# Kernel tuning notes

Hardware: AMD Instinct MI355X
Metric: run time of the kernel (lower is better)

Reference implementation:

```python
import jax, jax.numpy as jnp
import numpy as np
from jax import lax

B = 100000      # number of time steps (outer 'batch' loop in the torch code)
SEQ = 1         # inner seq_len
SPIN = 365      # spinLen
TRAIN = 50000   # traintimeLen


def setup_inputs() -> dict:
    key = jax.random.key(0)
    k1, k2, k3, k4, k5 = jax.random.split(key, 5)
    x = jax.random.uniform(k1, (B, SEQ, 2), dtype=jnp.float32)          # [batch, seq, 2] (batch_first)
    y_obs = jax.random.uniform(k2, (B, 1), dtype=jnp.float32)
    weight_r_yom = jax.random.uniform(k3, (1, 1), dtype=jnp.float32)
    weight_r_ylm = jax.random.uniform(k4, (1, 1), dtype=jnp.float32)
    weight_r_yfm = jax.random.uniform(k5, (1, 1), dtype=jnp.float32)
    return {"x": x, "y_obs": y_obs, "weight_r_yom": weight_r_yom,
            "weight_r_ylm": weight_r_ylm, "weight_r_yfm": weight_r_yfm,
            "epoch": 0, "time_lag": 0}


def reference(x, y_obs, weight_r_yom, weight_r_ylm, weight_r_yfm, epoch, time_lag):
    batch_size = x.shape[0]
    dtype = x.dtype
    # obs std over training window (torch.std is unbiased -> ddof=1)
    obsstd = jnp.std(y_obs[SPIN:TRAIN], ddof=1)

    # gates from softmax over the three scalar weights (constant over time)
    ew = jnp.exp(jnp.stack([weight_r_yom, weight_r_ylm, weight_r_yfm]))  # [3,1,1]
    denom = ew.sum(0)
    oo = ew[0] / denom   # (1,1) outflow gate
    ol = ew[1] / denom   # (1,1) loss (ET) gate

    def time_step(c0, u):
        # c0: (1,1) cell state; u: (2,) = (precip u1, PET u2)
        u1, u2 = u[0], u[1]
        safe_c = jnp.where(c0 > 0, c0, jnp.asarray(1.0, dtype))
        olc_raw = jnp.where(c0 > 0, ol - jax.nn.elu(ol - u2 / safe_c), ol)
        f = jax.nn.relu(1.0 - oo - olc_raw)          # forget gate uses pre-relu constraint
        olc = jax.nn.relu(olc_raw)
        c1 = f * c0 + u1                              # ib = 0 -> full input
        outs = (oo * c0, c0, ol * c0, olc * c0, olc, f)
        return c1, outs

    def batch_step(c0, u_seq):
        # u_seq: [SEQ, 2]; stored outputs correspond to the LAST inner t step
        c1, outs = lax.scan(time_step, c0, u_seq)
        return c1, tuple(o[-1] for o in outs)

    c_init = jnp.zeros((1, 1), dtype=dtype)
    _, (q, c, l, lc, g_olc, g_f) = lax.scan(batch_step, c_init, x[time_lag:])

    def pad(a):
        a = a.reshape(-1, 1)
        return jnp.concatenate([jnp.zeros((time_lag, 1), dtype), a], axis=0)

    h_n = pad(q)                     # bp = ib*g = 0, so h_n == q_n == oo*c0
    c_n = pad(c)
    l_n = pad(l)
    lc_n = pad(lc)
    Gate_olc = pad(g_olc)
    Gate_f = pad(g_f)

    tail = jnp.concatenate([jnp.zeros((time_lag, 1), dtype),
                            jnp.ones((batch_size - time_lag, 1), dtype)], axis=0)
    Gate_oo = oo[0, 0] * tail
    Gate_ol = ol[0, 0] * tail
    obs_std = obsstd * tail

    zeros = jnp.zeros((batch_size, 1), dtype)
    bp_n = zeros
    Gate_ib = zeros
    h_nout = jnp.concatenate([h_n, obs_std], axis=1)

    return (h_n, c_n, l_n, lc_n, bp_n, Gate_ib, Gate_oo, Gate_ol,
            Gate_olc, Gate_f, h_nout, obs_std)
```

## Files before the change

### kernel.cpp

```cpp
#include <hip/hip_runtime.h>
#include <math.h>

#define NB    100000
#define TRAIN 50000
#define SPIN  365
#define WARM  64
#define TPB   256
#define SCAN_BLKS ((NB + TPB - 1) / TPB)
#define RED_BLKS  64
#define WIN   (TPB + WARM)

#define V4_BASE  368
#define V4_COUNT 12408

__global__ __launch_bounds__(TPB) void k_all(const float* __restrict__ x,
                                             const float* __restrict__ y_obs,
                                             const float* __restrict__ w0,
                                             const float* __restrict__ w1,
                                             const float* __restrict__ w2,
                                             float* __restrict__ out) {
    const int tid = threadIdx.x;

    if (blockIdx.x < RED_BLKS) {
        __shared__ double ssum[TPB];
        __shared__ double ssq[TPB];
        const int b   = blockIdx.x;
        const int gid = b * TPB + tid;

        double s = 0.0, q = 0.0;
        if (gid < V4_COUNT) {
            const float4 v = ((const float4*)(y_obs + V4_BASE))[gid];
            s = (double)v.x + (double)v.y + (double)v.z + (double)v.w;
            q = (double)v.x * v.x + (double)v.y * v.y
              + (double)v.z * v.z + (double)v.w * v.w;
        }
        if (b == 0 && tid == 0) {
            for (int i = SPIN; i < V4_BASE; ++i) {
                double v = (double)y_obs[i];
                s += v; q += v * v;
            }
        }
        ssum[tid] = s;
        ssq[tid]  = q;
        __syncthreads();
        for (int off = TPB / 2; off > 0; off >>= 1) {
            if (tid < off) {
                ssum[tid] += ssum[tid + off];
                ssq[tid]  += ssq[tid + off];
            }
            __syncthreads();
        }
        __syncthreads();
        double fs = 0.0, fq = 0.0;
        {
            const float4* y4 = (const float4*)(y_obs + V4_BASE);
            for (int i = tid; i < V4_COUNT; i += TPB) {
                float4 v = y4[i];
                fs += (double)v.x + (double)v.y + (double)v.z + (double)v.w;
                fq += (double)v.x * v.x + (double)v.y * v.y
                    + (double)v.z * v.z + (double)v.w * v.w;
            }
            if (tid == 0) {
                for (int i = SPIN; i < V4_BASE; ++i) {
                    double v = (double)y_obs[i];
                    fs += v; fq += v * v;
                }
            }
        }
        __syncthreads();
        ssum[tid] = fs;
        ssq[tid]  = fq;
        __syncthreads();
        for (int off = TPB / 2; off > 0; off >>= 1) {
            if (tid < off) {
                ssum[tid] += ssum[tid + off];
                ssq[tid]  += ssq[tid + off];
            }
            __syncthreads();
        }
        const double n    = (double)(TRAIN - SPIN);
        const double mean = ssum[0] / n;
        const double var  = (ssq[0] - n * mean * mean) / (n - 1.0);
        const float  stdv = (float)sqrt(var);

        float* __restrict__ o_std = out + 12 * NB;
        float* __restrict__ o_hn  = out + 10 * NB;
        const int nth = RED_BLKS * TPB;
        for (int i = b * TPB + tid; i < NB; i += nth) {
            o_std[i]        = stdv;
            o_hn[2 * i + 1] = stdv;
        }
    } else {
        __shared__ float su1[WIN];
        __shared__ float su2[WIN];
        const int b = blockIdx.x - RED_BLKS;
        const int t = b * TPB + tid;

        float e0 = expf(w0[0]);
        float e1 = expf(w1[0]);
        float e2 = expf(w2[0]);
        float denom = e0 + e1 + e2;
        const float oo   = e0 / denom;
        const float ol   = e1 / denom;
        const float omoo = 1.0f - oo;

        const int w0i = max(0, b * TPB - WARM);
        const int r1  = min(NB, b * TPB + TPB);
        const int n4  = (r1 - w0i) >> 1;
        if (tid < n4) {
            const float4 v = ((const float4*)(((const float2*)x) + w0i))[tid];
            su1[2 * tid]     = v.x;  su2[2 * tid]     = v.y;
            su1[2 * tid + 1] = v.z;  su2[2 * tid + 1] = v.w;
        }
        __syncthreads();

        if (t >= NB) return;

        int   wstart = max(0, t - WARM);
        float c = (wstart == 0) ? 0.0f : 1.0f;
        for (int it = wstart; it < t; ++it) {
            float u1 = su1[it - w0i];
            float u2 = su2[it - w0i];
            float r  = __builtin_amdgcn_rcpf(c);
            float z  = ol - u2 * r;
            float el = (z > 0.0f) ? z : (__expf(z) - 1.0f);
            float praw    = ol - el;
            float olc_raw = (c > 0.0f) ? praw : ol;
            float f  = fmaxf(omoo - olc_raw, 0.0f);
            c = fmaf(f, c, u1);
        }
        float u2 = su2[t - w0i];
        float r  = __builtin_amdgcn_rcpf(c);
        float z  = ol - u2 * r;
        float el = (z > 0.0f) ? z : (__expf(z) - 1.0f);
        float praw    = ol - el;
        float olc_raw = (c > 0.0f) ? praw : ol;
        float f   = fmaxf(omoo - olc_raw, 0.0f);
        float olc = fmaxf(olc_raw, 0.0f);
        float h   = oo * c;

        out[0  * NB + t]     = h;
        out[1  * NB + t]     = c;
        out[2  * NB + t]     = ol * c;
        out[3  * NB + t]     = olc * c;
        out[4  * NB + t]     = 0.0f;
        out[5  * NB + t]     = 0.0f;
        out[6  * NB + t]     = oo;
        out[7  * NB + t]     = ol;
        out[8  * NB + t]     = olc;
        out[9  * NB + t]     = f;
        out[10 * NB + 2*t]   = h;
    }
}

extern "C" void kernel_launch(void* const* d_in, const int* in_sizes, int n_in,
                              void* d_out, int out_size, void* d_ws, size_t ws_size,
                              hipStream_t stream) {
    const float* x     = (const float*)d_in[0];
    const float* y_obs = (const float*)d_in[1];
    const float* w0    = (const float*)d_in[2];
    const float* w1    = (const float*)d_in[3];
    const float* w2    = (const float*)d_in[4];
    float* out = (float*)d_out;

    k_all<<<RED_BLKS + SCAN_BLKS, TPB, 0, stream>>>(x, y_obs, w0, w1, w2, out);
}
```

Baseline: 80.44 us.

## Split std reduction into per-block partials plus a finalize kernel

Before, each of the 64 reduction blocks redundantly re-read the whole training window to compute the full std, then wrote the std broadcast outputs. Now each block writes only its partial sum and sum of squares to workspace. A second kernel reduces the 64 partials with wavefront shuffles and writes the std columns. This removes the 64x redundant global reads and reductions but adds a second kernel launch and a dependency between the two kernels.

Result: faster. 73.90 us (-8.1%).

```diff
diff --git a/kernel.cpp b/kernel.cpp
--- a/kernel.cpp
+++ b/kernel.cpp
@@ -13,12 +13,14 @@
 #define V4_BASE  368
 #define V4_COUNT 12408
 
-__global__ __launch_bounds__(TPB) void k_all(const float* __restrict__ x,
-                                             const float* __restrict__ y_obs,
-                                             const float* __restrict__ w0,
-                                             const float* __restrict__ w1,
-                                             const float* __restrict__ w2,
-                                             float* __restrict__ out) {
+
+__global__ __launch_bounds__(TPB) void k_main(const float* __restrict__ x,
+                                              const float* __restrict__ y_obs,
+                                              const float* __restrict__ w0,
+                                              const float* __restrict__ w1,
+                                              const float* __restrict__ w2,
+                                              float* __restrict__ ws,
+                                              float* __restrict__ out) {
     const int tid = threadIdx.x;
 
     if (blockIdx.x < RED_BLKS) {
@@ -50,45 +52,10 @@
             }
             __syncthreads();
         }
-        __syncthreads();
-        double fs = 0.0, fq = 0.0;
-        {
-            const float4* y4 = (const float4*)(y_obs + V4_BASE);
-            for (int i = tid; i < V4_COUNT; i += TPB) {
-                float4 v = y4[i];
-                fs += (double)v.x + (double)v.y + (double)v.z + (double)v.w;
-                fq += (double)v.x * v.x + (double)v.y * v.y
-                    + (double)v.z * v.z + (double)v.w * v.w;
-            }
-            if (tid == 0) {
-                for (int i = SPIN; i < V4_BASE; ++i) {
-                    double v = (double)y_obs[i];
-                    fs += v; fq += v * v;
-                }
-            }
-        }
-        __syncthreads();
-        ssum[tid] = fs;
-        ssq[tid]  = fq;
-        __syncthreads();
-        for (int off = TPB / 2; off > 0; off >>= 1) {
-            if (tid < off) {
-                ssum[tid] += ssum[tid + off];
-                ssq[tid]  += ssq[tid + off];
-            }
-            __syncthreads();
-        }
-        const double n    = (double)(TRAIN - SPIN);
-        const double mean = ssum[0] / n;
-        const double var  = (ssq[0] - n * mean * mean) / (n - 1.0);
-        const float  stdv = (float)sqrt(var);
-
-        float* __restrict__ o_std = out + 12 * NB;
-        float* __restrict__ o_hn  = out + 10 * NB;
-        const int nth = RED_BLKS * TPB;
-        for (int i = b * TPB + tid; i < NB; i += nth) {
-            o_std[i]        = stdv;
-            o_hn[2 * i + 1] = stdv;
+        if (tid == 0) {
+            double* wsd = (double*)(ws + 8);
+            wsd[2 * b]     = ssum[0];
+            wsd[2 * b + 1] = ssq[0];
         }
     } else {
         __shared__ float su1[WIN];
@@ -139,18 +106,46 @@
         float olc = fmaxf(olc_raw, 0.0f);
         float h   = oo * c;
 
-        out[0  * NB + t]     = h;
-        out[1  * NB + t]     = c;
-        out[2  * NB + t]     = ol * c;
-        out[3  * NB + t]     = olc * c;
-        out[4  * NB + t]     = 0.0f;
-        out[5  * NB + t]     = 0.0f;
-        out[6  * NB + t]     = oo;
-        out[7  * NB + t]     = ol;
-        out[8  * NB + t]     = olc;
-        out[9  * NB + t]     = f;
-        out[10 * NB + 2*t]   = h;
+        out[0  * NB + t]   = h;
+        out[1  * NB + t]   = c;
+        out[2  * NB + t]   = ol * c;
+        out[3  * NB + t]   = olc * c;
+        out[4  * NB + t]   = 0.0f;
+        out[5  * NB + t]   = 0.0f;
+        out[6  * NB + t]   = oo;
+        out[7  * NB + t]   = ol;
+        out[8  * NB + t]   = olc;
+        out[9  * NB + t]   = f;
+        out[10 * NB + 2*t] = h;
     }
+}
+
+__global__ __launch_bounds__(TPB) void k_fin(const float* __restrict__ ws,
+                                             float* __restrict__ out) {
+    __shared__ float shs;
+    const int tid = threadIdx.x;
+    if (tid < 64) {
+        const double* wsd = (const double*)(ws + 8);
+        double s = wsd[2 * tid];
+        double q = wsd[2 * tid + 1];
+        for (int off = 32; off > 0; off >>= 1) {
+            s += __shfl_down(s, off, 64);
+            q += __shfl_down(q, off, 64);
+        }
+        if (tid == 0) {
+            double n    = (double)(TRAIN - SPIN);
+            double mean = s / n;
+            double var  = (q - n * mean * mean) / (n - 1.0);
+            shs = (float)sqrt(var);
+        }
+    }
+    __syncthreads();
+    const float stdv = shs;
+
+    const int i = blockIdx.x * TPB + tid;
+    if (i >= NB) return;
+    out[12 * NB + i]         = stdv;
+    out[10 * NB + 2 * i + 1] = stdv;
 }
 
 extern "C" void kernel_launch(void* const* d_in, const int* in_sizes, int n_in,
@@ -162,6 +157,8 @@
     const float* w1    = (const float*)d_in[3];
     const float* w2    = (const float*)d_in[4];
     float* out = (float*)d_out;
+    float* ws  = (float*)d_ws;
 
-    k_all<<<RED_BLKS + SCAN_BLKS, TPB, 0, stream>>>(x, y_obs, w0, w1, w2, out);
+    k_main<<<RED_BLKS + SCAN_BLKS, TPB, 0, stream>>>(x, y_obs, w0, w1, w2, ws, out);
+    k_fin<<<SCAN_BLKS, TPB, 0, stream>>>(ws, out);
 }
```
